# Kernel optimization log

Hardware: AMD Instinct MI355X
Metric: run time of the kernel (lower is better)

Reference implementation:

```python
import jax, jax.numpy as jnp
import numpy as np

IS = 256                 # image_size (nr.Renderer default)
NEAR, FAR = 0.1, 100.0   # renderer z clipping defaults
VIEW_ANGLE_DEG = 30.0    # renderer viewing_angle default
CAM_DIST, ELEV, AZIM = 2.732, 0.0, 90.0  # get_points_from_angles args in forward()
FACE_CHUNK = 128
EPS = 1e-9


def _eye():
    e, a = np.radians(ELEV), np.radians(AZIM)
    return jnp.array([CAM_DIST * np.cos(e) * np.sin(a),
                      CAM_DIST * np.sin(e),
                      -CAM_DIST * np.cos(e) * np.cos(a)], dtype=jnp.float32)


def _look_at(v, eye):
    # neural_renderer.look_at with at=origin, up=+y
    at = jnp.zeros(3, jnp.float32)
    up = jnp.array([0.0, 1.0, 0.0], jnp.float32)
    z = at - eye; z = z / jnp.linalg.norm(z)
    x = jnp.cross(up, z); x = x / jnp.linalg.norm(x)
    y = jnp.cross(z, x); y = y / jnp.linalg.norm(y)
    R = jnp.stack([x, y, z])           # [3,3] camera rotation
    return (v - eye) @ R.T


def _perspective(v, angle_deg):
    # neural_renderer.perspective: divide x,y by z*tan(viewing_angle)
    width = jnp.float32(np.tan(np.radians(angle_deg)))
    z = v[..., 2]
    return jnp.stack([v[..., 0] / (z * width), v[..., 1] / (z * width), z], -1)


def _pixel_grid():
    # pixel centers in NDC [-1,1]; row 0 = top of image (y decreasing)
    i = jnp.arange(IS, dtype=jnp.float32)
    xp = (2.0 * i + 1.0 - IS) / IS
    yp = (2.0 * (IS - 1.0 - i) + 1.0 - IS) / IS
    X, Y = jnp.meshgrid(xp, yp, indexing='xy')  # [IS(rows=y), IS(cols=x)]
    return X.reshape(-1), Y.reshape(-1)


def _silhouette(face_verts):
    # face_verts: [F,3,3] projected (x,y in NDC, z camera depth)
    xs, ys = _pixel_grid()                       # [P]
    F = face_verts.shape[0]
    fv = face_verts.reshape(F // FACE_CHUNK, FACE_CHUNK, 3, 3)

    def cover_chunk(fvc):                        # [Fc,3,3] -> [P] coverage
        x, y, z = fvc[:, :, 0], fvc[:, :, 1], fvc[:, :, 2]   # [Fc,3]
        x0, x1, x2 = x[:, 0], x[:, 1], x[:, 2]
        y0, y1, y2 = y[:, 0], y[:, 1], y[:, 2]
        denom = (y1 - y2) * (x0 - x2) + (x2 - x1) * (y0 - y2)  # [Fc]
        valid = jnp.abs(denom) > EPS
        d = jnp.where(valid, denom, 1.0)
        dx = xs[:, None] - x2[None, :]           # [P,Fc]
        dy = ys[:, None] - y2[None, :]
        w0 = ((y1 - y2)[None] * dx + (x2 - x1)[None] * dy) / d[None]
        w1 = ((y2 - y0)[None] * dx + (x0 - x2)[None] * dy) / d[None]
        w2 = 1.0 - w0 - w1
        inside = (w0 > 0) & (w1 > 0) & (w2 > 0) & valid[None]
        # perspective-correct depth at the pixel (as in NR's rasterizer)
        inv_z = w0 / z[None, :, 0] + w1 / z[None, :, 1] + w2 / z[None, :, 2]
        zp = 1.0 / inv_z
        cov = (inside & (zp > NEAR) & (zp < FAR)).astype(jnp.float32)
        return jnp.max(cov, axis=1)              # [P] float coverage of chunk

    covered = jnp.max(jax.lax.map(cover_chunk, fv), axis=0)  # [P]
    return covered.reshape(IS, IS)


def render_loss(vertices, image_ref, faces):
    v = vertices[0]                              # [V,3]
    v = _perspective(_look_at(v, _eye()), VIEW_ANGLE_DEG)
    fv = v[faces[0]]                             # [F,3,3] gather face vertices
    sil = _silhouette(fv)[None]                  # [1,IS,IS]
    return jnp.sum((sil - image_ref) ** 2)


def setup_inputs() -> dict:
    key = jax.random.key(0)
    k1, k2, k3 = jax.random.split(key, 3)
    V, F = 512, 1024
    vertices = 0.3 * jax.random.normal(k1, (1, V, 3), dtype=jnp.float32)
    faces = jax.random.randint(k2, (1, F, 3), 0, V, dtype=jnp.int32)
    image_ref = jax.random.uniform(k3, (1, IS, IS), dtype=jnp.float32)
    return {"vertices": vertices, "image_ref": image_ref, "faces": faces}


def reference(vertices, image_ref, faces):
    return render_loss(vertices, image_ref, faces)
```

## Files before the change

kernel.cpp:

```cpp
#include <hip/hip_runtime.h>


constexpr int NVERT = 512;
constexpr int QCAP  = 288;

__global__ __launch_bounds__(1024) void fused_k(
    const float* __restrict__ verts, const int* __restrict__ faces,
    const float* __restrict__ ref, float* __restrict__ out)
{
  __shared__ float sx[NVERT], sy[NVERT], sz[NVERT];
  __shared__ float L[4][QCAP][12];
  __shared__ int   cQ[4];
  __shared__ int   anyD;
  __shared__ unsigned long long smk[16];
  __shared__ float wsum[4];

  const int t    = threadIdx.x;
  const int lane = t & 63;
  const int w    = t >> 6;
  const int row  = blockIdx.x;
  const float ys = (2.0f*(255 - row) + 1.0f - 256.0f) * (1.0f/256.0f);

  if (t < 4)  cQ[t] = 0;
  if (t == 4) anyD = 0;

  const int i0 = faces[3*t], i1 = faces[3*t+1], i2 = faces[3*t+2];
  float X = 0.f, Y = 0.f, Z = 0.f;
  if (t < NVERT) { X = verts[3*t]; Y = verts[3*t+1]; Z = verts[3*t+2]; }

  if (t < NVERT) {
    float dx = X - 2.732f;
    float dy = Y;
    float dz = Z - (-1.6728675e-16f);
    const float r00 = 6.123234e-17f;
    float tx = dx*r00 + dz;
    float ty = dy;
    float tz = -dx + dz*r00;
    const float width = 0.57735026918962576f;
    float rzw = __builtin_amdgcn_rcpf(tz * width);
    sx[t] = tx * rzw;
    sy[t] = ty * rzw;
    sz[t] = tz;
  }
  __syncthreads();

  {
    float x0=sx[i0], y0=sy[i0], z0=sz[i0];
    float x1=sx[i1], y1=sy[i1], z1=sz[i1];
    float x2=sx[i2], y2=sy[i2], z2=sz[i2];

    float denom = (y1-y2)*(x0-x2) + (x2-x1)*(y0-y2);
    bool valid = fabsf(denom) > 1e-9f;
    float rd = __builtin_amdgcn_rcpf(valid ? denom : 1.0f);
    float a0=(y1-y2)*rd, b0=(x2-x1)*rd;
    float a1=(y2-y0)*rd, b1=(x0-x2)*rd;
    float c0 = -(a0*x2 + b0*y2);
    float c1 = -(a1*x2 + b1*y2);
    float rz0=__builtin_amdgcn_rcpf(z0);
    float rz1=__builtin_amdgcn_rcpf(z1);
    float rz2=__builtin_amdgcn_rcpf(z2);
    float dzA = rz0 - rz2, dzB = rz1 - rz2;
    float Az = a0*dzA + a1*dzB;
    float Bz = b0*dzA + b1*dzB;
    float Cz = c0*dzA + c1*dzB + rz2;

    float rzmin = fminf(rz0, fminf(rz1, rz2));
    float rzmax = fmaxf(rz0, fmaxf(rz1, rz2));
    float xmin = fminf(x0, fminf(x1, x2)), xmax = fmaxf(x0, fmaxf(x1, x2));
    float ymin = fminf(y0, fminf(y1, y2)), ymax = fmaxf(y0, fmaxf(y1, y2));
    bool passD = (rzmin > 0.01f) && (rzmax < 10.0f);
    bool failD = (rzmax <= 0.01f) || (rzmin >= 10.0f);
    bool rowHit = (ymin < ys) && (ymax > ys);
    bool alive = valid && rowHit && !failD;
    if (alive && !passD) anyD = 1;

#pragma unroll
    for (int q = 0; q < 4; ++q) {
      float qlo = (2.0f*(q*64)      + 1.0f - 256.0f) * (1.0f/256.0f);
      float qhi = (2.0f*(q*64 + 63) + 1.0f - 256.0f) * (1.0f/256.0f);
      bool want = alive && (xmin < qhi) && (xmax > qlo);
      unsigned long long m = __ballot((int)want);
      int cnt = __popcll(m);
      if (cnt) {
        int base = 0;
        if (lane == 0) base = atomicAdd(&cQ[q], cnt);
        base = __shfl(base, 0, 64);
        if (want) {
          int idx = base + __popcll(m & ((1ull << lane) - 1ull));
          if (idx < QCAP) {
            float* p = &L[q][idx][0];
            p[0]=a0; p[1]=b0; p[2]=c0; p[3]=a1; p[4]=b1; p[5]=c1;
            p[6]=Az; p[7]=Bz; p[8]=Cz;
          }
        }
      }
    }
  }
  __syncthreads();

  const int q = w & 3, chunk = w >> 2;
  const int n = min(cQ[q], QCAP);
  const float xs = (2.0f*(q*64 + lane) + 1.0f - 256.0f) * (1.0f/256.0f);
  bool covered = false;

  if (anyD == 0) {
    for (int i = chunk; i < n; i += 4) {
      const float* p = &L[q][i][0];
      float w0 = fmaf(p[0], xs, fmaf(p[1], ys, p[2]));
      float w1 = fmaf(p[3], xs, fmaf(p[4], ys, p[5]));
      covered |= (fminf(w0, w1) > 0.0f) & ((w0 + w1) < 1.0f);
    }
  } else {
    for (int i = chunk; i < n; i += 4) {
      const float* p = &L[q][i][0];
      float w0 = fmaf(p[0], xs, fmaf(p[1], ys, p[2]));
      float w1 = fmaf(p[3], xs, fmaf(p[4], ys, p[5]));
      float iz = fmaf(p[6], xs, fmaf(p[7], ys, p[8]));
      covered |= (fminf(w0, w1) > 0.0f) & ((w0 + w1) < 1.0f) &
                 (iz > 0.01f) & (iz < 10.0f);
    }
  }

  smk[w] = __ballot((int)covered);
  __syncthreads();

  if (t < 256) {
    int qq = t >> 6;
    unsigned long long mm = smk[qq] | smk[qq+4] | smk[qq+8] | smk[qq+12];
    float cv = (float)((mm >> (t & 63)) & 1ull);
    float diff = cv - ref[row*256 + t];
    float sq = diff * diff;
    for (int off = 32; off; off >>= 1) sq += __shfl_down(sq, off, 64);
    if ((t & 63) == 0) wsum[t >> 6] = sq;
  }
  __syncthreads();
  if (t == 0) atomicAdd(out, wsum[0] + wsum[1] + wsum[2] + wsum[3]);
}

extern "C" void kernel_launch(void* const* d_in, const int* in_sizes, int n_in,
                              void* d_out, int out_size, void* d_ws, size_t ws_size,
                              hipStream_t stream) {
  const float* verts = (const float*)d_in[0];
  const float* refim = (const float*)d_in[1];
  const int*   faces = (const int*)d_in[2];
  float* out = (float*)d_out;

  fused_k<<<256, 1024, 0, stream>>>(verts, faces, refim, out);
}
```

Before: 64.01 us.

## Process four image rows per block, sharing face setup across rows

Each block now handles four consecutive rows instead of one, with face setup and binning done once per four rows using a widened row band test. Each wave owns one row and column quarter and loops over every binned face, instead of four waves splitting the face list for a single pixel group. This removes the ballot merge step and cuts the repeated per-block vertex transform and face setup, but launches only 64 blocks, which may underfill the GPU. The wider band also puts more faces in each list, which risks overflowing QCAP.

```diff
diff --git a/kernel.cpp b/kernel.cpp
--- a/kernel.cpp
+++ b/kernel.cpp
@@ -12,14 +12,14 @@
   __shared__ float L[4][QCAP][12];
   __shared__ int   cQ[4];
   __shared__ int   anyD;
-  __shared__ unsigned long long smk[16];
-  __shared__ float wsum[4];
+  __shared__ float wsum[16];
 
   const int t    = threadIdx.x;
   const int lane = t & 63;
   const int w    = t >> 6;
-  const int row  = blockIdx.x;
-  const float ys = (2.0f*(255 - row) + 1.0f - 256.0f) * (1.0f/256.0f);
+  const int r0   = blockIdx.x << 2;
+  const float ysTop = (255.0f - 2.0f*r0)       * (1.0f/256.0f);
+  const float ysBot = (255.0f - 2.0f*(r0 + 3)) * (1.0f/256.0f);
 
   if (t < 4)  cQ[t] = 0;
   if (t == 4) anyD = 0;
@@ -70,7 +70,7 @@
     float ymin = fminf(y0, fminf(y1, y2)), ymax = fmaxf(y0, fmaxf(y1, y2));
     bool passD = (rzmin > 0.01f) && (rzmax < 10.0f);
     bool failD = (rzmax <= 0.01f) || (rzmin >= 10.0f);
-    bool rowHit = (ymin < ys) && (ymax > ys);
+    bool rowHit = (ymin < ysTop) && (ymax > ysBot);
     bool alive = valid && rowHit && !failD;
     if (alive && !passD) anyD = 1;
 
@@ -98,20 +98,22 @@
   }
   __syncthreads();
 
-  const int q = w & 3, chunk = w >> 2;
-  const int n = min(cQ[q], QCAP);
+  const int rsel = w >> 2, q = w & 3;
+  const int row  = r0 + rsel;
+  const int n    = min(cQ[q], QCAP);
+  const float ys = (255.0f - 2.0f*row) * (1.0f/256.0f);
   const float xs = (2.0f*(q*64 + lane) + 1.0f - 256.0f) * (1.0f/256.0f);
   bool covered = false;
 
   if (anyD == 0) {
-    for (int i = chunk; i < n; i += 4) {
+    for (int i = 0; i < n; ++i) {
       const float* p = &L[q][i][0];
       float w0 = fmaf(p[0], xs, fmaf(p[1], ys, p[2]));
       float w1 = fmaf(p[3], xs, fmaf(p[4], ys, p[5]));
       covered |= (fminf(w0, w1) > 0.0f) & ((w0 + w1) < 1.0f);
     }
   } else {
-    for (int i = chunk; i < n; i += 4) {
+    for (int i = 0; i < n; ++i) {
       const float* p = &L[q][i][0];
       float w0 = fmaf(p[0], xs, fmaf(p[1], ys, p[2]));
       float w1 = fmaf(p[3], xs, fmaf(p[4], ys, p[5]));
@@ -121,20 +123,18 @@
     }
   }
 
-  smk[w] = __ballot((int)covered);
+  float cv = covered ? 1.0f : 0.0f;
+  float diff = cv - ref[row*256 + q*64 + lane];
+  float sq = diff * diff;
+  for (int off = 32; off; off >>= 1) sq += __shfl_down(sq, off, 64);
+  if (lane == 0) wsum[w] = sq;
   __syncthreads();
-
-  if (t < 256) {
-    int qq = t >> 6;
-    unsigned long long mm = smk[qq] | smk[qq+4] | smk[qq+8] | smk[qq+12];
-    float cv = (float)((mm >> (t & 63)) & 1ull);
-    float diff = cv - ref[row*256 + t];
-    float sq = diff * diff;
-    for (int off = 32; off; off >>= 1) sq += __shfl_down(sq, off, 64);
-    if ((t & 63) == 0) wsum[t >> 6] = sq;
+  if (t == 0) {
+    float s = 0.f;
+#pragma unroll
+    for (int i = 0; i < 16; ++i) s += wsum[i];
+    atomicAdd(out, s);
   }
-  __syncthreads();
-  if (t == 0) atomicAdd(out, wsum[0] + wsum[1] + wsum[2] + wsum[3]);
 }
 
 extern "C" void kernel_launch(void* const* d_in, const int* in_sizes, int n_in,
@@ -145,5 +145,5 @@
   const int*   faces = (const int*)d_in[2];
   float* out = (float*)d_out;
 
-  fused_k<<<256, 1024, 0, stream>>>(verts, faces, refim, out);
+  fused_k<<<64, 1024, 0, stream>>>(verts, faces, refim, out);
 }
```

Result: slower. 78.95 us (+23.3%).
